# Kernel tuning notes

Measured on AMD Instinct MI355X. Metric: run time of the kernel, lower is better.

The kernel has to match this reference:

```python
import jax, jax.numpy as jnp
import numpy as np

EPS_NORM = 1e-4
EPS_LOG = 1e-6


def normed_weight(W):
    # W: [O, I, K] (K=1). normalize() over dims (1,2) per output channel,
    # with norm scaled by alpha = sqrt(O / (O*I*K)) = 1/sqrt(I*K), then
    # divided again by sqrt(I*K) in get_normed_weight (eval path).
    O, I, K = W.shape
    fan_in = I * K
    norm = jnp.sqrt(jnp.sum(jnp.square(W), axis=(1, 2), keepdims=True))  # [O,1,1]
    norm = EPS_NORM + norm / np.sqrt(fan_in)
    return (W / norm) / np.sqrt(fan_in)


def complex_log(x):
    real = jnp.log(jnp.maximum(jnp.abs(x), EPS_LOG))
    imag = jnp.where(x < 0, jnp.pi, 0.0).astype(real.dtype)
    return jax.lax.complex(real, imag)


def logcumsumexp_complex(z, axis=-1):
    # stable complex logcumsumexp via associative scan:
    # logaddexp(a, b) = m + log(exp(a-m) + exp(b-m)), m = max(Re a, Re b)
    def combine(a, b):
        m = jnp.maximum(a.real, b.real)
        mc = jax.lax.complex(m, jnp.zeros_like(m))
        return mc + jnp.log(jnp.exp(a - mc) + jnp.exp(b - mc))
    return jax.lax.associative_scan(combine, z, axis=axis)


def min_gru(h, g):
    # h, g: [B, C, L]; parallel log-space minGRU recurrence along L
    log_scale = 0.5 * jnp.log(1.0 / jnp.cosh(g) + 1.0)
    log_coeffs = -jax.nn.softplus(g) + log_scale                 # real
    log_values = (-jax.nn.softplus(-g) + log_scale) + complex_log(h)  # complex
    a_star = jnp.cumsum(log_coeffs, axis=-1)                     # real
    a_star_c = jax.lax.complex(a_star, jnp.zeros_like(a_star))
    log_h = a_star_c + logcumsumexp_complex(log_values - a_star_c, axis=-1)
    return jnp.exp(log_h).real


def scaled_cat(xs, axis):
    Ns = [x.shape[axis] for x in xs]
    scale = np.sqrt(np.mean(Ns))
    return scale * jnp.concatenate([x * n ** -0.5 for n, x in zip(Ns, xs)], axis=axis)


def setup_inputs() -> dict:
    key = jax.random.key(0)
    k1, k2 = jax.random.split(key)
    B, D, L = 8, 512, 8192
    x = jax.random.normal(k1, (B, D, L), dtype=jnp.float32)
    W = jax.random.normal(k2, (2 * D, D, 1), dtype=jnp.float32)  # Conv1d(dim, 2*dim, 1) weight
    return {"x": x, "W": W}


def reference(x, W):
    Wn = normed_weight(W)  # [2D, D, 1]
    fb = jnp.einsum('oi,bil->bol', Wn[:, :, 0], x)  # [B, 2D, L]
    fore, back = jnp.split(fb, 2, axis=1)
    h_f, g_f = jnp.split(fore, 2, axis=1)
    back_r = back[..., ::-1]
    h_b, g_b = jnp.split(back_r, 2, axis=1)
    out_f = min_gru(h_f, g_f)
    out_b = min_gru(h_b, g_b)[..., ::-1]
    return scaled_cat([out_f, out_b], axis=1)
```

## Files before the change

### kernel.cpp

```cpp
#include <hip/hip_runtime.h>
#include <math.h>
#include <stdint.h>

#define LSEQ 8192
#define DIN  512
#define NB   8
#define NO   1024

typedef __bf16 bf16x8 __attribute__((ext_vector_type(8)));
typedef float f32x16 __attribute__((ext_vector_type(16)));

__device__ __forceinline__ uint32_t pack_bf16_rne(float lo, float hi) {
    uint32_t ul = __builtin_bit_cast(uint32_t, lo);
    uint32_t uh = __builtin_bit_cast(uint32_t, hi);
    ul += 0x7FFFu + ((ul >> 16) & 1u);
    uh += 0x7FFFu + ((uh >> 16) & 1u);
    return (ul >> 16) | (uh & 0xFFFF0000u);
}
__device__ __forceinline__ float bf16_lo(uint32_t w) {
    return __builtin_bit_cast(float, w << 16);
}
__device__ __forceinline__ float bf16_hi(uint32_t w) {
    return __builtin_bit_cast(float, w & 0xFFFF0000u);
}

__device__ __forceinline__ void gl_lds16(const void* g, void* l) {
    __builtin_amdgcn_global_load_lds(
        (const __attribute__((address_space(1))) void*)g,
        (__attribute__((address_space(3))) void*)l, 16, 0, 0);
}

__global__ void norm_kernel(const float* __restrict__ W, uint32_t* __restrict__ Wnb) {
    const int o = blockIdx.x;
    const int lane = threadIdx.x;
    const float* row = W + (size_t)o * DIN;
    float4 v0 = *(const float4*)(row + lane * 4);
    float4 v1 = *(const float4*)(row + 256 + lane * 4);
    float s = v0.x * v0.x + v0.y * v0.y + v0.z * v0.z + v0.w * v0.w
            + v1.x * v1.x + v1.y * v1.y + v1.z * v1.z + v1.w * v1.w;
#pragma unroll
    for (int m = 32; m; m >>= 1) s += __shfl_xor(s, m, 64);
    const float sq = 22.62741699796952f;
    const float scale = 1.0f / ((1e-4f + sqrtf(s) / sq) * sq);
    uint2 w0, w1;
    w0.x = pack_bf16_rne(v0.x * scale, v0.y * scale);
    w0.y = pack_bf16_rne(v0.z * scale, v0.w * scale);
    w1.x = pack_bf16_rne(v1.x * scale, v1.y * scale);
    w1.y = pack_bf16_rne(v1.z * scale, v1.w * scale);
    *(uint2*)&Wnb[o * 256 + lane * 2] = w0;
    *(uint2*)&Wnb[o * 256 + 128 + lane * 2] = w1;
}

__global__ __launch_bounds__(256)
void xpack_kernel(const float* __restrict__ x, uint32_t* __restrict__ xp) {
    __shared__ uint32_t sT[32 * 132];
    const int t  = threadIdx.x;
    const int bx = blockIdx.x;
    const int b  = blockIdx.y;
    const int lt = bx >> 3;
    const int ch = bx & 7;

    const float* xb = x + (size_t)b * DIN * LSEQ + lt * 128;
#pragma unroll
    for (int j = 0; j < 4; ++j) {
        const int idx = j * 256 + t;
        const int k2l = idx >> 5;
        const int lg  = idx & 31;
        const float* r0 = xb + (size_t)(2 * (ch * 32 + k2l)) * LSEQ + lg * 4;
        float4 a = *(const float4*)r0;
        float4 c = *(const float4*)(r0 + LSEQ);
        uint4 wv;
        wv.x = pack_bf16_rne(a.x, c.x);
        wv.y = pack_bf16_rne(a.y, c.y);
        wv.z = pack_bf16_rne(a.z, c.z);
        wv.w = pack_bf16_rne(a.w, c.w);
        *(uint4*)&sT[k2l * 132 + lg * 4] = wv;
    }
    __syncthreads();
    uint32_t* ob = xp + ((size_t)(b * 64 + lt) * 128) * 256 + ch * 32;
#pragma unroll
    for (int j = 0; j < 4; ++j) {
        const int idx = j * 256 + t;
        const int lp  = idx >> 3;
        const int gq  = idx & 7;
        uint4 wv;
        wv.x = sT[(gq * 4 + 0) * 132 + lp];
        wv.y = sT[(gq * 4 + 1) * 132 + lp];
        wv.z = sT[(gq * 4 + 2) * 132 + lp];
        wv.w = sT[(gq * 4 + 3) * 132 + lp];
        *(uint4*)&ob[(size_t)lp * 256 + gq * 4] = wv;
    }
}

__global__ __launch_bounds__(256)
void gemm_kernel(const uint32_t* __restrict__ WnbW, const uint32_t* __restrict__ xp,
                 uint32_t* __restrict__ fbp) {
    __shared__ uint32_t sA[2][2048];
    __shared__ uint32_t sB[2][2048];

    const int tid  = threadIdx.x;
    const int lane = tid & 63;
    const int w    = tid >> 6;
    const int wm   = w & 1, wn = w >> 1;

    const int bx  = blockIdx.x;
    const int xcd = bx & 7;
    const int t   = bx >> 3;
    const int o0  = (t & 7) * 128;
    const int ltg = xcd + ((t >> 3) << 3);
    const int l0  = ltg * 128;
    const int b   = blockIdx.y;

    const int rsub = lane >> 2;
    const int ssub = (lane & 3) ^ (rsub & 3);
    const uint32_t* gA0 = WnbW + (size_t)(o0 + w * 32 + rsub) * 256 + ssub * 4;
    const uint32_t* gA1 = gA0 + (size_t)16 * 256;
    const uint32_t* xptb = xp + (size_t)(b * 64 + ltg) * 32768;
    const uint32_t* gB0 = xptb + (size_t)(w * 32 + rsub) * 256 + ssub * 4;
    const uint32_t* gB1 = gB0 + (size_t)16 * 256;

    f32x16 acc[2][2];
#pragma unroll
    for (int i = 0; i < 2; ++i)
#pragma unroll
        for (int j = 0; j < 2; ++j)
#pragma unroll
            for (int r = 0; r < 16; ++r) acc[i][j][r] = 0.f;

#define STAGE(it, bs)                                      \
    do {                                                   \
        gl_lds16(gA0 + (it) * 16, &sA[bs][w * 512]);       \
        gl_lds16(gA1 + (it) * 16, &sA[bs][w * 512 + 256]); \
        gl_lds16(gB0 + (it) * 16, &sB[bs][w * 512]);       \
        gl_lds16(gB1 + (it) * 16, &sB[bs][w * 512 + 256]); \
    } while (0)

    STAGE(0, 0);
#pragma unroll 2
    for (int it = 0; it < 16; ++it) {
        const int cb = it & 1;
        __syncthreads();
        if (it + 1 < 16) STAGE(it + 1, cb ^ 1);
        const uint32_t* cA = sA[cb];
        const uint32_t* cB = sB[cb];
#pragma unroll
        for (int kh = 0; kh < 2; ++kh) {
            const int q = kh * 2 + (lane >> 5);
            bf16x8 af[2], bfr[2];
#pragma unroll
            for (int ms = 0; ms < 2; ++ms) {
                const int m = wm * 64 + ms * 32 + (lane & 31);
                af[ms] = *(const bf16x8*)&cA[m * 16 + ((q ^ (m & 3)) << 2)];
            }
#pragma unroll
            for (int ns = 0; ns < 2; ++ns) {
                const int col = wn * 64 + ns * 32 + (lane & 31);
                bfr[ns] = *(const bf16x8*)&cB[col * 16 + ((q ^ (col & 3)) << 2)];
            }
#pragma unroll
            for (int ms = 0; ms < 2; ++ms)
#pragma unroll
                for (int ns = 0; ns < 2; ++ns)
                    acc[ms][ns] = __builtin_amdgcn_mfma_f32_32x32x16_bf16(
                        af[ms], bfr[ns], acc[ms][ns], 0, 0, 0);
        }
    }
#undef STAGE

    uint32_t* fbp_b = fbp + (size_t)b * 512 * LSEQ + l0;
#pragma unroll
    for (int ms = 0; ms < 2; ++ms)
#pragma unroll
        for (int ns = 0; ns < 2; ++ns) {
            const f32x16 a = acc[ms][ns];
            const int rb = o0 + wm * 64 + ms * 32 + 4 * (lane >> 5);
            const int cc = wn * 64 + ns * 32 + (lane & 31);
#pragma unroll
            for (int rp = 0; rp < 8; ++rp) {
                const int r = rp * 2;
                const int row = rb + (r & 3) + 8 * (r >> 2);
                fbp_b[(size_t)(row >> 1) * LSEQ + cc] = pack_bf16_rne(a[r], a[r + 1]);
            }
        }
}

__global__ __launch_bounds__(512)
void scan_kernel(const uint32_t* __restrict__ fbp, float* __restrict__ out) {
    __shared__ uint32_t sbuf[8][2048];
    __shared__ float sA0[8], sB0[8], sA1[8], sB1[8];

    const int bx  = blockIdx.x;
    const int b   = blockIdx.y;
    const int dir = bx >> 7;
    const int p   = bx & 127;
    const int o2h = dir * 256 + p;
    const int o2g = dir * 256 + 128 + p;

    const int t    = threadIdx.x;
    const int lane = t & 63;
    const int w    = t >> 6;

    const uint32_t* hwp = fbp + ((size_t)b * 512 + o2h) * LSEQ + w * 1024;
    const uint32_t* gwp = fbp + ((size_t)b * 512 + o2g) * LSEQ + w * 1024;
    uint32_t* sw = sbuf[w];
    float* swf = (float*)sbuf[w];

#pragma unroll
    for (int i = 0; i < 4; ++i) {
        uint4 v = *(const uint4*)(hwp + i * 256 + lane * 4);
        const uint32_t g = i * 64 + lane;
        const uint32_t gs = g ^ ((g >> 3) & 7);
        *(uint4*)&sw[gs * 4] = v;
    }
#pragma unroll
    for (int i = 0; i < 4; ++i) {
        uint4 v = *(const uint4*)(gwp + i * 256 + lane * 4);
        const uint32_t g = i * 64 + lane;
        const uint32_t gs = g ^ ((g >> 3) & 7);
        *(uint4*)&sw[1024 + gs * 4] = v;
    }
    asm volatile("s_waitcnt lgkmcnt(0)" ::: "memory");

    float av0[16], vv0[16], av1[16], vv1[16];
#pragma unroll
    for (int q = 0; q < 4; ++q) {
        const uint32_t g = lane * 4 + q;
        const uint32_t gs = g ^ ((g >> 3) & 7);
        uint4 hw4 = *(const uint4*)&sw[gs * 4];
        uint4 gw4 = *(const uint4*)&sw[1024 + gs * 4];
        const uint32_t hws[4] = {hw4.x, hw4.y, hw4.z, hw4.w};
        const uint32_t gws[4] = {gw4.x, gw4.y, gw4.z, gw4.w};
#pragma unroll
        for (int s = 0; s < 4; ++s) {
            const int mo = q * 4 + s;
            {
                float g_ = fminf(fmaxf(bf16_lo(gws[s]), -30.f), 30.f);
                float eg = __expf(g_);
                float a  = rsqrtf(fmaf(eg, eg, 1.f));
                float h_ = bf16_lo(hws[s]);
                av0[mo] = a;
                vv0[mo] = a * eg * copysignf(fmaxf(fabsf(h_), 1e-6f), h_);
            }
            {
                float g_ = fminf(fmaxf(bf16_hi(gws[s]), -30.f), 30.f);
                float eg = __expf(g_);
                float a  = rsqrtf(fmaf(eg, eg, 1.f));
                float h_ = bf16_hi(hws[s]);
                av1[mo] = a;
                vv1[mo] = a * eg * copysignf(fmaxf(fabsf(h_), 1e-6f), h_);
            }
        }
    }

    float A0 = 1.f, B0 = 0.f, A1 = 1.f, B1 = 0.f;
    if (dir == 0) {
#pragma unroll
        for (int i = 0; i < 16; ++i) {
            B0 = fmaf(av0[i], B0, vv0[i]); A0 *= av0[i];
            B1 = fmaf(av1[i], B1, vv1[i]); A1 *= av1[i];
        }
    } else {
#pragma unroll
        for (int i = 15; i >= 0; --i) {
            B0 = fmaf(av0[i], B0, vv0[i]); A0 *= av0[i];
            B1 = fmaf(av1[i], B1, vv1[i]); A1 *= av1[i];
        }
    }

    if (dir == 0) {
#pragma unroll
        for (int off = 1; off < 64; off <<= 1) {
            float Ap0 = __shfl_up(A0, (unsigned)off, 64), Bp0 = __shfl_up(B0, (unsigned)off, 64);
            float Ap1 = __shfl_up(A1, (unsigned)off, 64), Bp1 = __shfl_up(B1, (unsigned)off, 64);
            if (lane >= off) {
                B0 = fmaf(A0, Bp0, B0); A0 *= Ap0;
                B1 = fmaf(A1, Bp1, B1); A1 *= Ap1;
            }
        }
        if (lane == 63) { sA0[w] = A0; sB0[w] = B0; sA1[w] = A1; sB1[w] = B1; }
    } else {
#pragma unroll
        for (int off = 1; off < 64; off <<= 1) {
            float Ap0 = __shfl_down(A0, (unsigned)off, 64), Bp0 = __shfl_down(B0, (unsigned)off, 64);
            float Ap1 = __shfl_down(A1, (unsigned)off, 64), Bp1 = __shfl_down(B1, (unsigned)off, 64);
            if (lane + off < 64) {
                B0 = fmaf(A0, Bp0, B0); A0 *= Ap0;
                B1 = fmaf(A1, Bp1, B1); A1 *= Ap1;
            }
        }
        if (lane == 0) { sA0[w] = A0; sB0[w] = B0; sA1[w] = A1; sB1[w] = B1; }
    }
    __syncthreads();
    float WB0 = 0.f, WB1 = 0.f;
    if (dir == 0) {
        for (int wv = 0; wv < w; ++wv) {
            WB0 = fmaf(sA0[wv], WB0, sB0[wv]);
            WB1 = fmaf(sA1[wv], WB1, sB1[wv]);
        }
    } else {
        for (int wv = 7; wv > w; --wv) {
            WB0 = fmaf(sA0[wv], WB0, sB0[wv]);
            WB1 = fmaf(sA1[wv], WB1, sB1[wv]);
        }
    }
    float eA0, eB0, eA1, eB1;
    if (dir == 0) {
        eA0 = __shfl_up(A0, 1u, 64); eB0 = __shfl_up(B0, 1u, 64);
        eA1 = __shfl_up(A1, 1u, 64); eB1 = __shfl_up(B1, 1u, 64);
        if (lane == 0) { eA0 = 1.f; eB0 = 0.f; eA1 = 1.f; eB1 = 0.f; }
    } else {
        eA0 = __shfl_down(A0, 1u, 64); eB0 = __shfl_down(B0, 1u, 64);
        eA1 = __shfl_down(A1, 1u, 64); eB1 = __shfl_down(B1, 1u, 64);
        if (lane == 63) { eA0 = 1.f; eB0 = 0.f; eA1 = 1.f; eB1 = 0.f; }
    }
    float H0 = fmaf(eA0, WB0, eB0);
    float H1 = fmaf(eA1, WB1, eB1);

    if (dir == 0) {
#pragma unroll
        for (int i = 0; i < 16; ++i) {
            H0 = fmaf(av0[i], H0, vv0[i]); vv0[i] = H0;
            H1 = fmaf(av1[i], H1, vv1[i]); vv1[i] = H1;
        }
    } else {
#pragma unroll
        for (int i = 15; i >= 0; --i) {
            H0 = fmaf(av0[i], H0, vv0[i]); vv0[i] = H0;
            H1 = fmaf(av1[i], H1, vv1[i]); vv1[i] = H1;
        }
    }

#pragma unroll
    for (int q = 0; q < 4; ++q) {
        const uint32_t g = lane * 4 + q;
        const uint32_t gs = g ^ ((g >> 3) & 7);
        *(float4*)&swf[gs * 4] =
            make_float4(vv0[q * 4], vv0[q * 4 + 1], vv0[q * 4 + 2], vv0[q * 4 + 3]);
        *(float4*)&swf[1024 + gs * 4] =
            make_float4(vv1[q * 4], vv1[q * 4 + 1], vv1[q * 4 + 2], vv1[q * 4 + 3]);
    }
    asm volatile("s_waitcnt lgkmcnt(0)" ::: "memory");
    const int c0 = 2 * p, c1 = 2 * p + 1;
    float* orow0 = out + ((size_t)b * 512 + dir * 256 + c0) * LSEQ + w * 1024;
    float* orow1 = out + ((size_t)b * 512 + dir * 256 + c1) * LSEQ + w * 1024;
#pragma unroll
    for (int i = 0; i < 4; ++i) {
        const uint32_t g = i * 64 + lane;
        const uint32_t gs = g ^ ((g >> 3) & 7);
        *(float4*)(orow0 + i * 256 + lane * 4) = *(const float4*)&swf[gs * 4];
        *(float4*)(orow1 + i * 256 + lane * 4) = *(const float4*)&swf[1024 + gs * 4];
    }
}

extern "C" void kernel_launch(void* const* d_in, const int* in_sizes, int n_in,
                              void* d_out, int out_size, void* d_ws, size_t ws_size,
                              hipStream_t stream) {
    const float* x = (const float*)d_in[0];
    const float* W = (const float*)d_in[1];
    float* out = (float*)d_out;

    uint32_t* Wnb = (uint32_t*)d_ws;
    uint32_t* fbp = (uint32_t*)((char*)d_ws + (size_t)NO * DIN * 2);
    uint32_t* xp  = (uint32_t*)((char*)d_ws + (size_t)NO * DIN * 2
                                + (size_t)NB * 512 * LSEQ * 4);

    norm_kernel<<<dim3(NO), dim3(64), 0, stream>>>(W, Wnb);
    xpack_kernel<<<dim3(512, NB), dim3(256), 0, stream>>>(x, xp);
    gemm_kernel<<<dim3(512, NB), dim3(256), 0, stream>>>((const uint32_t*)Wnb, xp, fbp);
    scan_kernel<<<dim3(256, NB), dim3(512), 0, stream>>>(fbp, out);
}
```

Baseline: 365.0 us.

## Pre-tile W and x into MFMA fragment order for contiguous LDS staging

The norm and xpack kernels now write the bf16 weight and activation buffers in a blocked layout that matches the per-iteration LDS tile and the MFMA fragment order. The GEMM can then stage each k-step with fully contiguous 16-byte global-to-LDS loads and read fragments without XOR swizzle address arithmetic. This is meant to improve global load coalescing and simplify LDS addressing. The trade-off is that the unswizzled LDS reads may introduce bank conflicts, and the producer kernels' stores become more scattered.

```diff
diff --git a/kernel.cpp b/kernel.cpp
--- a/kernel.cpp
+++ b/kernel.cpp
@@ -29,6 +29,7 @@
         (const __attribute__((address_space(1))) void*)g,
         (__attribute__((address_space(3))) void*)l, 16, 0, 0);
 }
+
 
 __global__ void norm_kernel(const float* __restrict__ W, uint32_t* __restrict__ Wnb) {
     const int o = blockIdx.x;
@@ -47,8 +48,13 @@
     w0.y = pack_bf16_rne(v0.z * scale, v0.w * scale);
     w1.x = pack_bf16_rne(v1.x * scale, v1.y * scale);
     w1.y = pack_bf16_rne(v1.z * scale, v1.w * scale);
-    *(uint2*)&Wnb[o * 256 + lane * 2] = w0;
-    *(uint2*)&Wnb[o * 256 + 128 + lane * 2] = w1;
+    const int ot = o >> 7, mb = (o >> 5) & 3, m31 = o & 31;
+    const int it0 = lane >> 3;
+    const int q   = (lane >> 1) & 3;
+    const int wic = (lane & 1) * 2;
+    uint32_t* base = Wnb + (size_t)ot * 32768 + ((mb * 4 + q) * 32 + m31) * 4 + wic;
+    *(uint2*)&base[(size_t)it0 * 2048] = w0;
+    *(uint2*)&base[(size_t)(it0 + 8) * 2048] = w1;
 }
 
 __global__ __launch_bounds__(256)
@@ -77,7 +83,7 @@
         *(uint4*)&sT[k2l * 132 + lg * 4] = wv;
     }
     __syncthreads();
-    uint32_t* ob = xp + ((size_t)(b * 64 + lt) * 128) * 256 + ch * 32;
+    uint32_t* ob = xp + (size_t)(b * 64 + lt) * 32768;
 #pragma unroll
     for (int j = 0; j < 4; ++j) {
         const int idx = j * 256 + t;
@@ -88,12 +94,15 @@
         wv.y = sT[(gq * 4 + 1) * 132 + lp];
         wv.z = sT[(gq * 4 + 2) * 132 + lp];
         wv.w = sT[(gq * 4 + 3) * 132 + lp];
-        *(uint4*)&ob[(size_t)lp * 256 + gq * 4] = wv;
+        const int itl   = ch * 2 + (gq >> 2);
+        const int q     = gq & 3;
+        const int chunk = ((lp >> 5) * 4 + q) * 32 + (lp & 31);
+        *(uint4*)&ob[(size_t)itl * 2048 + chunk * 4] = wv;
     }
 }
 
 __global__ __launch_bounds__(256)
-void gemm_kernel(const uint32_t* __restrict__ WnbW, const uint32_t* __restrict__ xp,
+void gemm_kernel(const uint32_t* __restrict__ Wnb, const uint32_t* __restrict__ xp,
                  uint32_t* __restrict__ fbp) {
     __shared__ uint32_t sA[2][2048];
     __shared__ uint32_t sB[2][2048];
@@ -106,18 +115,14 @@
     const int bx  = blockIdx.x;
     const int xcd = bx & 7;
     const int t   = bx >> 3;
-    const int o0  = (t & 7) * 128;
+    const int o0t = t & 7;
+    const int o0  = o0t * 128;
     const int ltg = xcd + ((t >> 3) << 3);
     const int l0  = ltg * 128;
     const int b   = blockIdx.y;
 
-    const int rsub = lane >> 2;
-    const int ssub = (lane & 3) ^ (rsub & 3);
-    const uint32_t* gA0 = WnbW + (size_t)(o0 + w * 32 + rsub) * 256 + ssub * 4;
-    const uint32_t* gA1 = gA0 + (size_t)16 * 256;
-    const uint32_t* xptb = xp + (size_t)(b * 64 + ltg) * 32768;
-    const uint32_t* gB0 = xptb + (size_t)(w * 32 + rsub) * 256 + ssub * 4;
-    const uint32_t* gB1 = gB0 + (size_t)16 * 256;
+    const uint32_t* gA = Wnb + (size_t)o0t * 32768 + (w * 2) * 256 + lane * 4;
+    const uint32_t* gB = xp + (size_t)(b * 64 + ltg) * 32768 + (w * 2) * 256 + lane * 4;
 
     f32x16 acc[2][2];
 #pragma unroll
@@ -127,12 +132,12 @@
 #pragma unroll
             for (int r = 0; r < 16; ++r) acc[i][j][r] = 0.f;
 
-#define STAGE(it, bs)                                      \
-    do {                                                   \
-        gl_lds16(gA0 + (it) * 16, &sA[bs][w * 512]);       \
-        gl_lds16(gA1 + (it) * 16, &sA[bs][w * 512 + 256]); \
-        gl_lds16(gB0 + (it) * 16, &sB[bs][w * 512]);       \
-        gl_lds16(gB1 + (it) * 16, &sB[bs][w * 512 + 256]); \
+#define STAGE(it, bs)                                               \
+    do {                                                            \
+        gl_lds16(gA + (size_t)(it) * 2048, &sA[bs][w * 512]);       \
+        gl_lds16(gA + (size_t)(it) * 2048 + 256, &sA[bs][w * 512 + 256]); \
+        gl_lds16(gB + (size_t)(it) * 2048, &sB[bs][w * 512]);       \
+        gl_lds16(gB + (size_t)(it) * 2048 + 256, &sB[bs][w * 512 + 256]); \
     } while (0)
 
     STAGE(0, 0);
@@ -145,18 +150,13 @@
         const uint32_t* cB = sB[cb];
 #pragma unroll
         for (int kh = 0; kh < 2; ++kh) {
-            const int q = kh * 2 + (lane >> 5);
             bf16x8 af[2], bfr[2];
 #pragma unroll
-            for (int ms = 0; ms < 2; ++ms) {
-                const int m = wm * 64 + ms * 32 + (lane & 31);
-                af[ms] = *(const bf16x8*)&cA[m * 16 + ((q ^ (m & 3)) << 2)];
-            }
-#pragma unroll
-            for (int ns = 0; ns < 2; ++ns) {
-                const int col = wn * 64 + ns * 32 + (lane & 31);
-                bfr[ns] = *(const bf16x8*)&cB[col * 16 + ((q ^ (col & 3)) << 2)];
-            }
+            for (int ms = 0; ms < 2; ++ms)
+                af[ms] = *(const bf16x8*)&cA[((wm * 2 + ms) * 4 + kh * 2) * 128 + lane * 4];
+#pragma unroll
+            for (int ns = 0; ns < 2; ++ns)
+                bfr[ns] = *(const bf16x8*)&cB[((wn * 2 + ns) * 4 + kh * 2) * 128 + lane * 4];
 #pragma unroll
             for (int ms = 0; ms < 2; ++ms)
 #pragma unroll
@@ -366,6 +366,6 @@
 
     norm_kernel<<<dim3(NO), dim3(64), 0, stream>>>(W, Wnb);
     xpack_kernel<<<dim3(512, NB), dim3(256), 0, stream>>>(x, xp);
-    gemm_kernel<<<dim3(512, NB), dim3(256), 0, stream>>>((const uint32_t*)Wnb, xp, fbp);
+    gemm_kernel<<<dim3(512, NB), dim3(256), 0, stream>>>(Wnb, xp, fbp);
     scan_kernel<<<dim3(256, NB), dim3(512), 0, stream>>>(fbp, out);
 }
```

Result: faster. 350.1 us (-4.1%).
